# Kernel optimization log

Measured on AMD Instinct MI355X. Metric: run time of the kernel, lower is better.

## Reference

```python
import jax, jax.numpy as jnp
import numpy as np

N_NODES = 10000
N_EDGES = 160000
N_HEADS = 2
N_IN = 16   # fc input dim = x channels (15) + 1 dist channel
N_OUT = 32
ALPHA = 0.2
B, T_LEN = 2, 8


def setup_inputs() -> dict:
    key = jax.random.key(0)
    ks = jax.random.split(key, 6)
    x = jax.random.normal(ks[0], (B, T_LEN, N_NODES, N_IN - 1), dtype=jnp.float32)
    d_ew = jax.random.uniform(ks[1], (N_EDGES + N_NODES, N_HEADS), dtype=jnp.float32)
    u_edges = jax.random.randint(ks[2], (N_EDGES, 2), 0, N_NODES, dtype=jnp.int64)
    u_dist = jax.random.uniform(ks[3], (N_EDGES,), dtype=jnp.float32)
    W = jax.random.normal(ks[4], (N_OUT, N_IN), dtype=jnp.float32) * (1.0 / np.sqrt(N_IN))
    b = jax.random.normal(ks[5], (N_OUT,), dtype=jnp.float32) * 0.01
    return {"x": x, "T": T_LEN, "d_ew": d_ew, "u_edges": u_edges,
            "u_dist": u_dist, "W": W, "b": b}


def reference(x, T, d_ew, u_edges, u_dist, W, b):
    # d_edges = [u_edges; self-loops], d_dist = [u_dist; zeros]
    loops = jnp.arange(N_NODES, dtype=u_edges.dtype)
    d_edges = jnp.concatenate([u_edges, jnp.stack([loops, loops], axis=1)], axis=0)
    d_dist = jnp.concatenate([u_dist, jnp.zeros((N_NODES,), dtype=u_dist.dtype)], axis=0)
    node_i, node_j = d_edges[:, 0], d_edges[:, 1]

    Bx, t, _, C = x.shape
    # graph convolution: out[:, :, j] = sum_e{j(e)=j} d_ew[e] * x[:, :, i(e)]
    xg = x[:, :, node_i, :]                               # (B, t, E, C)
    msgs = xg[..., None, :] * d_ew[None, None, :, :, None]  # (B, t, E, H, C)
    x_conv = jnp.zeros((Bx, t, N_NODES, N_HEADS, C), dtype=x.dtype)
    x_conv = x_conv.at[:, :, node_j].add(msgs)            # (B, t, N, H, C)

    # dist convolution: (N, H)
    dist_conv = jnp.zeros((N_NODES, N_HEADS), dtype=d_ew.dtype)
    dist_conv = dist_conv.at[node_j].add(d_dist[:, None] * d_ew)

    # concat dist channel, broadcast over (B, t)
    dist_b = jnp.broadcast_to(dist_conv[None, None, :, :, None],
                              (Bx, t, N_NODES, N_HEADS, 1))
    x_feature = jnp.concatenate([x_conv, dist_b], axis=-1)  # (B, t, N, H, C+1)

    x_out = jnp.einsum('btnhc,oc->btnho', x_feature, W) + b

    # temporal alpha-blend (RHS uses pre-update values, as in torch slice assign)
    x_out = jnp.concatenate(
        [x_out[:, :1], ALPHA * x_out[:, :-1] + (1.0 - ALPHA) * x_out[:, 1:]], axis=1)
    return jax.nn.sigmoid(x_out)
```

## Files before the change

### kernel.cpp

```cpp
#include <hip/hip_runtime.h>
#include <hip/hip_bf16.h>

#define NN 10000
#define NE 160000
#define NBT 16
#define CIN 15
#define HPAD 128
#define BCAP 64
#define NOUT 32
#define ALPHA_F 0.2f

#define TRANS_BLKS 625
#define EDGE_BLKS  625

__device__ __forceinline__ float bf2f(unsigned short u) {
    return __uint_as_float(((unsigned int)u) << 16);
}
__device__ __forceinline__ unsigned short f2bf(float f) {
    __hip_bfloat16 h = __float2bfloat16(f);
    return *(unsigned short*)&h;
}

__global__ __launch_bounds__(256) void zero_ws(int* __restrict__ p) {
    int i = blockIdx.x * 256 + threadIdx.x;
    if (i < NN) p[i] = 0;
}

__global__ __launch_bounds__(256) void prep(const float* __restrict__ x,
                                            const int* __restrict__ edges,
                                            const float* __restrict__ dist,
                                            const float* __restrict__ dew,
                                            unsigned short* __restrict__ xh,
                                            int* __restrict__ cursor,
                                            int2* __restrict__ epay) {
    __shared__ float tile[NBT][16 * CIN];
    int bid = blockIdx.x;
    int tid = threadIdx.x;
    if (bid < TRANS_BLKS) {
        int n0 = bid * 16;
        if (tid < 16 * CIN) {
#pragma unroll
            for (int bt = 0; bt < NBT; ++bt)
                tile[bt][tid] = x[((size_t)bt * NN + n0) * CIN + tid];
        }
        __syncthreads();
        for (int g = tid; g < 16 * 256; g += 256) {
            int ln = g >> 8;
            int r  = g & 255;
            int c  = r & 15;
            int bt = r >> 4;
            float v = (c < 15) ? tile[bt][ln * CIN + c] : 0.f;
            xh[(size_t)(n0 + ln) * 256 + r] = f2bf(v);
        }
    } else {
        int e = (bid - TRANS_BLKS) * 256 + tid;
        if (e < NE) {
            int2 ed = ((const int2*)edges)[e];
            float2 w = ((const float2*)dew)[e];
            float d = dist[e];
            int pos = atomicAdd(&cursor[ed.y], 1);
            if (pos < BCAP) {
                unsigned int px = (unsigned int)ed.x | ((unsigned int)f2bf(d) << 16);
                unsigned int py = (unsigned int)f2bf(w.x) | ((unsigned int)f2bf(w.y) << 16);
                epay[ed.y * BCAP + pos] = make_int2((int)px, (int)py);
            }
        }
    }
}

__global__ __launch_bounds__(256) void fused_node(const unsigned short* __restrict__ xh,
                                                  const int* __restrict__ cursor,
                                                  const int2* __restrict__ epay,
                                                  const float* __restrict__ dew,
                                                  const float* __restrict__ W,
                                                  const float* __restrict__ bias,
                                                  float* __restrict__ out) {
    __shared__ float s_xc[4][2][HPAD];

    const int tid = threadIdx.x;
    const int unit = tid >> 6;
    const int lane = tid & 63;
    const int bid = blockIdx.x;
    const int hf = (bid & 7) >> 2;
    const int gidHalf = (bid >> 3) * 4 + (bid & 3);
    const int n = gidHalf * 4 + unit;
    const int o = lane & 31;
    const int h = lane >> 5;
    const bool ispad = (lane & 7) == 7;

    float4 w0_ = *(const float4*)(W + o * 16);
    float4 w1_ = *(const float4*)(W + o * 16 + 4);
    float4 w2_ = *(const float4*)(W + o * 16 + 8);
    float4 w3_ = *(const float4*)(W + o * 16 + 12);
    float bo = bias[o];

    int deg = cursor[n];
    if (deg > BCAP) deg = BCAP;

    int2 pay = epay[n * BCAP + (lane & 31)];

    const char* xbase = (const char*)xh + hf * 256 + 4 * lane;
    float a00 = 0.f, a01 = 0.f, a10 = 0.f, a11 = 0.f;

    int dmain = deg > 32 ? 32 : deg;
#pragma unroll 8
    for (int k = 0; k < dmain; ++k) {
        int sx = __builtin_amdgcn_readlane(pay.x, k);
        int sw = __builtin_amdgcn_readlane(pay.y, k);
        unsigned int u = *(const unsigned int*)(xbase + (size_t)((sx & 0xFFFF) << 9));
        float w0 = __uint_as_float((unsigned int)sw << 16);
        float w1 = __uint_as_float((unsigned int)sw & 0xFFFF0000u);
        float de = __uint_as_float((unsigned int)sx & 0xFFFF0000u);
        float x0 = __uint_as_float(u << 16);
        float x1 = ispad ? de : __uint_as_float(u & 0xFFFF0000u);
        a00 += w0 * x0; a01 += w0 * x1;
        a10 += w1 * x0; a11 += w1 * x1;
    }
    if (deg > 32) {
        int2 pay2 = epay[n * BCAP + 32 + (lane & 31)];
        for (int k = 32; k < deg; ++k) {
            int sx = __builtin_amdgcn_readlane(pay2.x, k - 32);
            int sw = __builtin_amdgcn_readlane(pay2.y, k - 32);
            unsigned int u = *(const unsigned int*)(xbase + (size_t)((sx & 0xFFFF) << 9));
            float w0 = __uint_as_float((unsigned int)sw << 16);
            float w1 = __uint_as_float((unsigned int)sw & 0xFFFF0000u);
            float de = __uint_as_float((unsigned int)sx & 0xFFFF0000u);
            float x0 = __uint_as_float(u << 16);
            float x1 = ispad ? de : __uint_as_float(u & 0xFFFF0000u);
            a00 += w0 * x0; a01 += w0 * x1;
            a10 += w1 * x0; a11 += w1 * x1;
        }
    }
    {
        unsigned int u = *(const unsigned int*)(xbase + ((size_t)n << 9));
        float w0 = dew[2 * (NE + n) + 0];
        float w1 = dew[2 * (NE + n) + 1];
        float x0 = __uint_as_float(u << 16);
        float x1 = __uint_as_float(u & 0xFFFF0000u);
        a00 += w0 * x0; a01 += w0 * x1;
        a10 += w1 * x0; a11 += w1 * x1;
    }
    *(float2*)&s_xc[unit][0][2 * lane] = make_float2(a00, a01);
    *(float2*)&s_xc[unit][1][2 * lane] = make_float2(a10, a11);

    asm volatile("s_waitcnt lgkmcnt(0)" ::: "memory");

    {
        float Wr[16] = { w0_.x, w0_.y, w0_.z, w0_.w,
                         w1_.x, w1_.y, w1_.z, w1_.w,
                         w2_.x, w2_.y, w2_.z, w2_.w,
                         w3_.x, w3_.y, w3_.z, w3_.w };
        const float* xc = s_xc[unit][h];
        float prev = 0.f;
#pragma unroll
        for (int t = 0; t < 8; ++t) {
            const float* xt = xc + t * 16;
            float4 v0 = *(const float4*)(xt);
            float4 v1 = *(const float4*)(xt + 4);
            float4 v2 = *(const float4*)(xt + 8);
            float4 v3 = *(const float4*)(xt + 12);
            float y = bo;
            y += Wr[0]*v0.x + Wr[1]*v0.y + Wr[2]*v0.z + Wr[3]*v0.w;
            y += Wr[4]*v1.x + Wr[5]*v1.y + Wr[6]*v1.z + Wr[7]*v1.w;
            y += Wr[8]*v2.x + Wr[9]*v2.y + Wr[10]*v2.z + Wr[11]*v2.w;
            y += Wr[12]*v3.x + Wr[13]*v3.y + Wr[14]*v3.z + Wr[15]*v3.w;
            float v = (t == 0) ? y : (ALPHA_F * prev + (1.f - ALPHA_F) * y);
            float sg = 1.f / (1.f + __expf(-v));
            __builtin_nontemporal_store(sg,
                &out[(((size_t)(hf * 8 + t) * NN + n) * 2 + h) * NOUT + o]);
            prev = y;
        }
    }
}

extern "C" void kernel_launch(void* const* d_in, const int* in_sizes, int n_in,
                              void* d_out, int out_size, void* d_ws, size_t ws_size,
                              hipStream_t stream) {
    const float* x     = (const float*)d_in[0];
    const float* dew   = (const float*)d_in[2];
    const int*   edges = (const int*)d_in[3];
    const float* dist  = (const float*)d_in[4];
    const float* W     = (const float*)d_in[5];
    const float* bias  = (const float*)d_in[6];
    float* out = (float*)d_out;

    unsigned short* xh = (unsigned short*)d_ws;
    int2* epay   = (int2*)(xh + (size_t)NN * 256);
    int* cursor  = (int*)(epay + (size_t)NN * BCAP);

    zero_ws<<<(NN + 255) / 256, 256, 0, stream>>>(cursor);
    prep<<<TRANS_BLKS + EDGE_BLKS, 256, 0, stream>>>(x, edges, dist, dew,
                                                     xh, cursor, epay);
    fused_node<<<5000, 256, 0, stream>>>(xh, cursor, epay, dew, W, bias, out);
}
```

Before: 53.27 us.

## Split node gather across half-waves with wider bf16 loads and cross-half reduction

The per-node edge gather is reorganised so each half-wave handles alternate edges. Each lane now loads four bf16 channels at once instead of two, and the two halves' partial sums are combined with a shuffle-xor. This roughly halves the serial gather iterations per node and widens each memory access, aiming to shorten the latency-bound dependency chain. In exchange it adds ds_bpermute shuffles in place of scalar readlane, predication for odd degrees, and a final cross-lane reduction.

```diff
diff --git a/kernel.cpp b/kernel.cpp
--- a/kernel.cpp
+++ b/kernel.cpp
@@ -13,13 +13,12 @@
 #define TRANS_BLKS 625
 #define EDGE_BLKS  625
 
-__device__ __forceinline__ float bf2f(unsigned short u) {
-    return __uint_as_float(((unsigned int)u) << 16);
-}
 __device__ __forceinline__ unsigned short f2bf(float f) {
     __hip_bfloat16 h = __float2bfloat16(f);
     return *(unsigned short*)&h;
 }
+__device__ __forceinline__ float bfl(unsigned int u) { return __uint_as_float(u << 16); }
+__device__ __forceinline__ float bfh(unsigned int u) { return __uint_as_float(u & 0xFFFF0000u); }
 
 __global__ __launch_bounds__(256) void zero_ws(int* __restrict__ p) {
     int i = blockIdx.x * 256 + threadIdx.x;
@@ -80,13 +79,15 @@
     const int tid = threadIdx.x;
     const int unit = tid >> 6;
     const int lane = tid & 63;
+    const int sub = lane & 31;
+    const int grp = lane >> 5;
     const int bid = blockIdx.x;
     const int hf = (bid & 7) >> 2;
     const int gidHalf = (bid >> 3) * 4 + (bid & 3);
     const int n = gidHalf * 4 + unit;
     const int o = lane & 31;
     const int h = lane >> 5;
-    const bool ispad = (lane & 7) == 7;
+    const bool ispad = (sub & 3) == 3;
 
     float4 w0_ = *(const float4*)(W + o * 16);
     float4 w1_ = *(const float4*)(W + o * 16 + 4);
@@ -96,52 +97,67 @@
 
     int deg = cursor[n];
     if (deg > BCAP) deg = BCAP;
-
-    int2 pay = epay[n * BCAP + (lane & 31)];
-
-    const char* xbase = (const char*)xh + hf * 256 + 4 * lane;
-    float a00 = 0.f, a01 = 0.f, a10 = 0.f, a11 = 0.f;
+    const int2* bucket = epay + n * BCAP;
+
+    int2 pay = bucket[sub + grp];
+
+    const char* xlane = (const char*)xh + hf * 256 + 8 * sub;
+    float ac0[4] = {0, 0, 0, 0};
+    float ac1[4] = {0, 0, 0, 0};
 
     int dmain = deg > 32 ? 32 : deg;
-#pragma unroll 8
-    for (int k = 0; k < dmain; ++k) {
-        int sx = __builtin_amdgcn_readlane(pay.x, k);
-        int sw = __builtin_amdgcn_readlane(pay.y, k);
-        unsigned int u = *(const unsigned int*)(xbase + (size_t)((sx & 0xFFFF) << 9));
-        float w0 = __uint_as_float((unsigned int)sw << 16);
-        float w1 = __uint_as_float((unsigned int)sw & 0xFFFF0000u);
-        float de = __uint_as_float((unsigned int)sx & 0xFFFF0000u);
-        float x0 = __uint_as_float(u << 16);
-        float x1 = ispad ? de : __uint_as_float(u & 0xFFFF0000u);
-        a00 += w0 * x0; a01 += w0 * x1;
-        a10 += w1 * x0; a11 += w1 * x1;
+    int pairs = (dmain + 1) >> 1;
+#pragma unroll 4
+    for (int i = 0; i < pairs; ++i) {
+        int sx = __shfl(pay.x, 2 * i, 32);
+        int sw = __shfl(pay.y, 2 * i, 32);
+        bool val = (2 * i + grp) < deg;
+        unsigned int su = (unsigned int)sx & 0x3FFFu;
+        uint2 u = *(const uint2*)(xlane + ((size_t)su << 9));
+        float w0 = val ? bfh((unsigned int)sw << 16) : 0.f;
+        float w1 = val ? bfh((unsigned int)sw) : 0.f;
+        float de = bfh((unsigned int)sx);
+        float x0 = bfl(u.x), x1 = bfh(u.x), x2 = bfl(u.y);
+        float x3 = ispad ? de : bfh(u.y);
+        ac0[0] += w0 * x0; ac0[1] += w0 * x1; ac0[2] += w0 * x2; ac0[3] += w0 * x3;
+        ac1[0] += w1 * x0; ac1[1] += w1 * x1; ac1[2] += w1 * x2; ac1[3] += w1 * x3;
     }
     if (deg > 32) {
-        int2 pay2 = epay[n * BCAP + 32 + (lane & 31)];
-        for (int k = 32; k < deg; ++k) {
-            int sx = __builtin_amdgcn_readlane(pay2.x, k - 32);
-            int sw = __builtin_amdgcn_readlane(pay2.y, k - 32);
-            unsigned int u = *(const unsigned int*)(xbase + (size_t)((sx & 0xFFFF) << 9));
-            float w0 = __uint_as_float((unsigned int)sw << 16);
-            float w1 = __uint_as_float((unsigned int)sw & 0xFFFF0000u);
-            float de = __uint_as_float((unsigned int)sx & 0xFFFF0000u);
-            float x0 = __uint_as_float(u << 16);
-            float x1 = ispad ? de : __uint_as_float(u & 0xFFFF0000u);
-            a00 += w0 * x0; a01 += w0 * x1;
-            a10 += w1 * x0; a11 += w1 * x1;
-        }
+        int2 payB = bucket[32 + sub + grp];
+        int pairsB = (deg - 32 + 1) >> 1;
+        for (int i = 0; i < pairsB; ++i) {
+            int sx = __shfl(payB.x, 2 * i, 32);
+            int sw = __shfl(payB.y, 2 * i, 32);
+            bool val = (32 + 2 * i + grp) < deg;
+            unsigned int su = (unsigned int)sx & 0x3FFFu;
+            uint2 u = *(const uint2*)(xlane + ((size_t)su << 9));
+            float w0 = val ? bfh((unsigned int)sw << 16) : 0.f;
+            float w1 = val ? bfh((unsigned int)sw) : 0.f;
+            float de = bfh((unsigned int)sx);
+            float x0 = bfl(u.x), x1 = bfh(u.x), x2 = bfl(u.y);
+            float x3 = ispad ? de : bfh(u.y);
+            ac0[0] += w0 * x0; ac0[1] += w0 * x1; ac0[2] += w0 * x2; ac0[3] += w0 * x3;
+            ac1[0] += w1 * x0; ac1[1] += w1 * x1; ac1[2] += w1 * x2; ac1[3] += w1 * x3;
+        }
+    }
+#pragma unroll
+    for (int j = 0; j < 4; ++j) {
+        ac0[j] += __shfl_xor(ac0[j], 32, 64);
+        ac1[j] += __shfl_xor(ac1[j], 32, 64);
     }
     {
-        unsigned int u = *(const unsigned int*)(xbase + ((size_t)n << 9));
+        uint2 u = *(const uint2*)(xlane + ((size_t)n << 9));
         float w0 = dew[2 * (NE + n) + 0];
         float w1 = dew[2 * (NE + n) + 1];
-        float x0 = __uint_as_float(u << 16);
-        float x1 = __uint_as_float(u & 0xFFFF0000u);
-        a00 += w0 * x0; a01 += w0 * x1;
-        a10 += w1 * x0; a11 += w1 * x1;
-    }
-    *(float2*)&s_xc[unit][0][2 * lane] = make_float2(a00, a01);
-    *(float2*)&s_xc[unit][1][2 * lane] = make_float2(a10, a11);
+        float xs[4] = { bfl(u.x), bfh(u.x), bfl(u.y), bfh(u.y) };
+#pragma unroll
+        for (int j = 0; j < 4; ++j) { ac0[j] += w0 * xs[j]; ac1[j] += w1 * xs[j]; }
+    }
+    {
+        float v0 = grp ? ac1[0] : ac0[0], v1 = grp ? ac1[1] : ac0[1];
+        float v2 = grp ? ac1[2] : ac0[2], v3 = grp ? ac1[3] : ac0[3];
+        *(float4*)&s_xc[unit][grp][4 * sub] = make_float4(v0, v1, v2, v3);
+    }
 
     asm volatile("s_waitcnt lgkmcnt(0)" ::: "memory");
 
```

After: 49.25 us. 1.08x faster.
